# Kernel optimization log

Hardware: AMD Instinct MI355X
Metric: run time of the kernel (lower is better)

The kernel has to match this reference:

```python
import jax, jax.numpy as jnp
import numpy as np

N = 50000        # num nodes
E = 800000       # num edges (before self loops)
IN = 128         # in_channels
HID = 64         # hidden_channels
HEADS = 3        # num_heads
OUT = 32         # out_channels
SLOPE = 0.2      # PyG GATConv default negative_slope
HC = HEADS * HID


def setup_inputs() -> dict:
    key = jax.random.key(0)
    ks = jax.random.split(key, 12)

    def glorot(k, shape, fan_in):
        return jax.random.normal(k, shape, dtype=jnp.float32) / np.float32(np.sqrt(fan_in))

    x = jax.random.normal(ks[0], (N, IN), dtype=jnp.float32)
    edge_index = jax.random.randint(ks[1], (2, E), 0, N, dtype=jnp.int32)
    return {
        "x": x,
        "edge_index": edge_index,
        "W1": glorot(ks[2], (IN, HC), IN),
        "a_src1": glorot(ks[3], (HEADS, HID), HID),
        "a_dst1": glorot(ks[4], (HEADS, HID), HID),
        "b1": jnp.zeros((HC,), jnp.float32),
        "W2": glorot(ks[5], (HC, HC), HC),
        "a_src2": glorot(ks[6], (HEADS, HID), HID),
        "a_dst2": glorot(ks[7], (HEADS, HID), HID),
        "b2": jnp.zeros((HC,), jnp.float32),
        "Wf1": glorot(ks[8], (HC, 64), HC),
        "bf1": jnp.zeros((64,), jnp.float32),
        "Wf2": glorot(ks[9], (64, OUT), 64),
        "bf2": jnp.zeros((OUT,), jnp.float32),
        "num_nodes": N,
    }


def gat_conv(x, src, dst, W, a_src, a_dst, b, num_nodes):
    """PyG-style GATConv: linear -> edge score (LeakyReLU) -> segment softmax
    over incoming edges per destination -> weighted scatter-sum -> concat heads."""
    H, C = a_src.shape
    h = (x @ W).reshape(num_nodes, H, C)              # [N,H,C]
    alpha_s = jnp.einsum("nhc,hc->nh", h, a_src)      # [N,H]
    alpha_d = jnp.einsum("nhc,hc->nh", h, a_dst)      # [N,H]
    e = jax.nn.leaky_relu(alpha_s[src] + alpha_d[dst], SLOPE)  # [E',H]
    # numerically stable segment softmax over destination nodes
    m = jax.lax.stop_gradient(jax.ops.segment_max(e, dst, num_segments=num_nodes))
    ex = jnp.exp(e - m[dst])
    denom = jax.ops.segment_sum(ex, dst, num_segments=num_nodes)
    alpha = ex / (denom[dst] + 1e-16)                 # [E',H]
    msg = h[src] * alpha[:, :, None]                  # [E',H,C]
    out = jax.ops.segment_sum(msg, dst, num_segments=num_nodes)  # [N,H,C]
    return out.reshape(num_nodes, H * C) + b


def reference(x, edge_index, W1, a_src1, a_dst1, b1, W2, a_src2, a_dst2, b2,
              Wf1, bf1, Wf2, bf2, num_nodes):
    # add self loops (PyG GATConv default)
    loops = jnp.arange(num_nodes, dtype=edge_index.dtype)
    src = jnp.concatenate([edge_index[0], loops])
    dst = jnp.concatenate([edge_index[1], loops])

    h = gat_conv(x, src, dst, W1, a_src1, a_dst1, b1, num_nodes)
    h = jax.nn.elu(h)
    # dropout is identity in eval mode
    h = gat_conv(h, src, dst, W2, a_src2, a_dst2, b2, num_nodes)
    h = jax.nn.elu(h)
    h = h @ Wf1 + bf1
    return h @ Wf2 + bf2
```

## Files before the change

kernel.cpp:

```cpp
#include <hip/hip_runtime.h>

#define N_NODES 50000
#define E_EDGES 800000
#define EP (E_EDGES + N_NODES)
#define IN_CH 128
#define HID 64
#define HEADS 3
#define HC 192
#define OUT_CH 32
#define SLOPE 0.2f

#define N4 12500
#define SCAN_BLK 49

#define MB_W1 96
#define MB_W2 (MB_W1 + 144)
#define MB_FOLD (MB_W2 + 25)
#define MB_HIST (MB_FOLD + 3321)

typedef __attribute__((ext_vector_type(8))) short bf16x8;
typedef __attribute__((ext_vector_type(4))) float f32x4;

__device__ __forceinline__ unsigned short f2bf(float f) {
    unsigned int u = __float_as_uint(f);
    u = (u + 0x7fffu + ((u >> 16) & 1u)) >> 16;
    return (unsigned short)u;
}
__device__ __forceinline__ float loF(unsigned int u) { return __uint_as_float(u << 16); }
__device__ __forceinline__ float hiF(unsigned int u) { return __uint_as_float(u & 0xFFFF0000u); }

__device__ __forceinline__ unsigned int fkey(float f) {
    unsigned int u = __float_as_uint(f);
    return (u & 0x80000000u) ? ~u : (u | 0x80000000u);
}
__device__ __forceinline__ float unfkey(unsigned int k) {
    unsigned int u = (k & 0x80000000u) ? (k ^ 0x80000000u) : ~k;
    return __uint_as_float(u);
}


__global__ __launch_bounds__(256) void mega_pre_kernel(
    const float* __restrict__ W1, unsigned short* __restrict__ W1T,
    const float* __restrict__ W2, unsigned short* __restrict__ W2T,
    const float* __restrict__ Wf1, const float* __restrict__ bf1,
    const float* __restrict__ Wf2, const float* __restrict__ bf2,
    unsigned short* __restrict__ WfTb, float* __restrict__ bf,
    const int* __restrict__ ei, int* __restrict__ cnt) {
    int b = blockIdx.x, t = threadIdx.x;
    if (b < MB_W1) {
        int k = (b & 3) * 32 + (t & 31);
        int n = (b >> 2) * 8 + (t >> 5);
        W1T[n * IN_CH + k] = f2bf(W1[(size_t)k * HC + n]);
    } else if (b < MB_W2) {
        int bb = b - MB_W1;
        int k = (bb % 6) * 32 + (t & 31);
        int n = (bb / 6) * 8 + (t >> 5);
        W2T[n * HC + k] = f2bf(W2[(size_t)k * HC + n]);
    } else if (b < MB_FOLD) {
        int id = (b - MB_W2) * 256 + t;
        if (id < HC * OUT_CH) {
            int i = id / OUT_CH, j = id % OUT_CH;
            float s = 0.f;
            for (int k = 0; k < 64; ++k) s += Wf1[i * 64 + k] * Wf2[k * OUT_CH + j];
            WfTb[j * HC + i] = f2bf(s);
        } else if (id < HC * OUT_CH + OUT_CH) {
            int j = id - HC * OUT_CH;
            float s = bf2[j];
            for (int k = 0; k < 64; ++k) s += bf1[k] * Wf2[k * OUT_CH + j];
            bf[j] = s;
        }
    } else {
        int i = (b - MB_FOLD) * 256 + t;
        if (i < EP) {
            int d = (i < E_EDGES) ? ei[E_EDGES + i] : (i - E_EDGES);
            atomicAdd(&cnt[d], 1);
        }
    }
}


__global__ __launch_bounds__(256) void scan_local_kernel(int* __restrict__ cnt,
                                                         int* __restrict__ offs,
                                                         int* __restrict__ bsum) {
    __shared__ int s[256];
    int t = threadIdx.x;
    int g = blockIdx.x * 256 + t;
    int4 v = make_int4(0, 0, 0, 0);
    if (g < N4) v = ((const int4*)cnt)[g];
    int sum = v.x + v.y + v.z + v.w;
    s[t] = sum; __syncthreads();
    #pragma unroll
    for (int o = 1; o < 256; o <<= 1) {
        int u = (t >= o) ? s[t - o] : 0;
        __syncthreads();
        s[t] += u;
        __syncthreads();
    }
    int ex = s[t] - sum;
    if (g < N4) {
        int4 w;
        w.x = ex;
        w.y = ex + v.x;
        w.z = ex + v.x + v.y;
        w.w = ex + v.x + v.y + v.z;
        ((int4*)offs)[g] = w;
        ((int4*)cnt)[g] = make_int4(0, 0, 0, 0);
    }
    if (t == 255) bsum[blockIdx.x] = s[255];
}

__global__ __launch_bounds__(256) void scan_add_kernel(int* __restrict__ offs,
                                                       const int* __restrict__ bsum) {
    int lane = threadIdx.x & 63;
    int orig = (lane < SCAN_BLK) ? bsum[lane] : 0;
    int v = orig;
    #pragma unroll
    for (int o = 1; o < 64; o <<= 1) {
        int u = __shfl_up(v, o);
        if (lane >= o) v += u;
    }
    int add = __shfl(v, blockIdx.x) - __shfl(orig, blockIdx.x);
    int total = __shfl(v, SCAN_BLK - 1);
    int g = blockIdx.x * 256 + threadIdx.x;
    if (g < N4) {
        int4 w = ((int4*)offs)[g];
        w.x += add; w.y += add; w.z += add; w.w += add;
        ((int4*)offs)[g] = w;
    }
    if (blockIdx.x == 0 && threadIdx.x == 0) offs[N_NODES] = total;
}

__global__ void scatter_kernel(const int* __restrict__ ei, const int* __restrict__ offs,
                               int* __restrict__ cnt, int* __restrict__ src_sort) {
    int i = blockIdx.x * 256 + threadIdx.x;
    if (i >= EP) return;
    int s_, d_;
    if (i < E_EDGES) { s_ = ei[i]; d_ = ei[E_EDGES + i]; }
    else             { s_ = d_ = i - E_EDGES; }
    int slot = atomicAdd(&cnt[d_], 1);
    src_sort[offs[d_] + slot] = s_;
}


#define GBM 128
#define GBK 64
#define LDA 72
#define CS_STR 200

template <int K, bool XF32>
__global__ __launch_bounds__(256) void gemm_mfma_kernel(
    const float* __restrict__ Af, const unsigned short* __restrict__ Ab,
    const unsigned short* __restrict__ Wt,
    const float* __restrict__ a_src, const float* __restrict__ a_dst,
    unsigned short* __restrict__ Hb, float* __restrict__ AS, float* __restrict__ AD,
    unsigned int* __restrict__ mk) {
    __shared__ __align__(16) unsigned char smem[51200];
    __shared__ float pmx[4][3];
    unsigned short (*As)[LDA] = (unsigned short (*)[LDA])smem;
    unsigned short (*Bs)[LDA] = (unsigned short (*)[LDA])(smem + GBM * LDA * 2);
    int tid = threadIdx.x;
    int wid = tid >> 6, lane = tid & 63;
    int l15 = lane & 15, l4 = lane >> 4;
    int m0 = blockIdx.x * GBM;
    int sr = tid >> 3, sc = (tid & 7) * 8;

    f32x4 acc[2][12];
    #pragma unroll
    for (int m = 0; m < 2; ++m)
        #pragma unroll
        for (int n = 0; n < 12; ++n) acc[m][n] = (f32x4){0.f, 0.f, 0.f, 0.f};

    for (int kb = 0; kb < K; kb += GBK) {
        #pragma unroll
        for (int i = 0; i < 4; ++i) {
            int r = sr + 32 * i, grow = m0 + r;
            uint4 v = make_uint4(0, 0, 0, 0);
            if (XF32) {
                if (grow < N_NODES) {
                    const float* xp = Af + (size_t)grow * K + kb + sc;
                    float4 v0 = *(const float4*)xp;
                    float4 v1 = *(const float4*)(xp + 4);
                    v.x = (unsigned int)f2bf(v0.x) | ((unsigned int)f2bf(v0.y) << 16);
                    v.y = (unsigned int)f2bf(v0.z) | ((unsigned int)f2bf(v0.w) << 16);
                    v.z = (unsigned int)f2bf(v1.x) | ((unsigned int)f2bf(v1.y) << 16);
                    v.w = (unsigned int)f2bf(v1.z) | ((unsigned int)f2bf(v1.w) << 16);
                }
            } else {
                if (grow < N_NODES) v = *(const uint4*)&Ab[(size_t)grow * K + kb + sc];
            }
            *(uint4*)&As[r][sc] = v;
        }
        #pragma unroll
        for (int i = 0; i < 6; ++i) {
            int n = sr + 32 * i;
            uint4 v = *(const uint4*)&Wt[(size_t)n * K + kb + sc];
            *(uint4*)&Bs[n][sc] = v;
        }
        __syncthreads();
        #pragma unroll
        for (int ks = 0; ks < 2; ++ks) {
            int ko = ks * 32 + l4 * 8;
            bf16x8 a0 = *(const bf16x8*)&As[wid * 32 + l15][ko];
            bf16x8 a1 = *(const bf16x8*)&As[wid * 32 + 16 + l15][ko];
            #pragma unroll
            for (int n = 0; n < 12; ++n) {
                bf16x8 b = *(const bf16x8*)&Bs[n * 16 + l15][ko];
                acc[0][n] = __builtin_amdgcn_mfma_f32_16x16x32_bf16(a0, b, acc[0][n], 0, 0, 0);
                acc[1][n] = __builtin_amdgcn_mfma_f32_16x16x32_bf16(a1, b, acc[1][n], 0, 0, 0);
            }
        }
        __syncthreads();
    }

    float asv[12], adv[12];
    #pragma unroll
    for (int n = 0; n < 12; ++n) {
        asv[n] = a_src[n * 16 + l15];
        adv[n] = a_dst[n * 16 + l15];
    }
    float pm[3] = {-1e30f, -1e30f, -1e30f};
    #pragma unroll
    for (int m = 0; m < 2; ++m)
        #pragma unroll
        for (int r = 0; r < 4; ++r) {
            float ps[3], pd[3];
            #pragma unroll
            for (int h = 0; h < 3; ++h) {
                float s = 0.f, d = 0.f;
                #pragma unroll
                for (int j = 0; j < 4; ++j) {
                    float v = acc[m][4 * h + j][r];
                    s += v * asv[4 * h + j];
                    d += v * adv[4 * h + j];
                }
                #pragma unroll
                for (int o = 1; o < 16; o <<= 1) { s += __shfl_xor(s, o); d += __shfl_xor(d, o); }
                ps[h] = s; pd[h] = d;
                pm[h] = fmaxf(pm[h], s);
            }
            if (l15 == 0) {
                int grow = m0 + wid * 32 + m * 16 + l4 * 4 + r;
                if (grow < N_NODES) {
                    #pragma unroll
                    for (int h = 0; h < 3; ++h) {
                        AS[grow * 3 + h] = ps[h];
                        AD[grow * 3 + h] = pd[h];
                    }
                }
            }
        }
    #pragma unroll
    for (int h = 0; h < 3; ++h) {
        pm[h] = fmaxf(pm[h], __shfl_xor(pm[h], 16));
        pm[h] = fmaxf(pm[h], __shfl_xor(pm[h], 32));
    }
    if (lane == 0) { pmx[wid][0] = pm[0]; pmx[wid][1] = pm[1]; pmx[wid][2] = pm[2]; }

    unsigned short* Cw = (unsigned short*)smem + wid * 32 * CS_STR;
    #pragma unroll
    for (int m = 0; m < 2; ++m)
        #pragma unroll
        for (int n = 0; n < 12; ++n)
            #pragma unroll
            for (int r = 0; r < 4; ++r)
                Cw[(m * 16 + l4 * 4 + r) * CS_STR + n * 16 + l15] = f2bf(acc[m][n][r]);
    __syncthreads();
    #pragma unroll
    for (int i = 0; i < 12; ++i) {
        int c = lane + 64 * i;
        int row = c / 24, off = c % 24;
        int grow = m0 + wid * 32 + row;
        if (grow < N_NODES) {
            uint4 v = *(const uint4*)&Cw[row * CS_STR + off * 8];
            *(uint4*)&Hb[(size_t)grow * HC + off * 8] = v;
        }
    }
    if (tid < 3) {
        float bm = fmaxf(fmaxf(pmx[0][tid], pmx[1][tid]), fmaxf(pmx[2][tid], pmx[3][tid]));
        atomicMax(&mk[tid], fkey(bm));
    }
}


__global__ __launch_bounds__(256) void aggregate_kernel(
    const int* __restrict__ src_sort, const int* __restrict__ offs,
    const float* __restrict__ AS, const float* __restrict__ AD,
    const unsigned int* __restrict__ mkey,
    const unsigned short* __restrict__ Hb, const float* __restrict__ bias,
    unsigned short* __restrict__ Aout) {
    int w = blockIdx.x * 4 + (threadIdx.x >> 6);
    int lane = threadIdx.x & 63;
    int g = lane >> 4, l = lane & 15;
    int beg = offs[w], end = offs[w + 1];

    float ad = 0.f, m = 0.f;
    if (l < 3) {
        ad = AD[w * 3 + l];
        float sm = unfkey(mkey[l]) + ad;
        m = fmaxf(sm, SLOPE * sm);
    }

    int c0 = l * 12;
    int h0 = c0 >> 6, h1 = (c0 + 4) >> 6, h2 = (c0 + 8) >> 6;
    float A0 = 0.f, A1 = 0.f, A2 = 0.f, A3 = 0.f;
    float B0 = 0.f, B1 = 0.f, B2 = 0.f, B3 = 0.f;
    float C0 = 0.f, C1 = 0.f, C2 = 0.f, C3 = 0.f;
    float den = 0.f;

    int p = beg + g;
    bool pv = p < end;
    int s_ = src_sort[pv ? p : (end - 1)];
    float e_;
    {
        float v = (l < 3) ? (AS[s_ * 3 + l] + ad) : 0.f;
        v = fmaxf(v, SLOPE * v);
        e_ = (pv && l < 3) ? __expf(v - m) : 0.f;
    }
    for (int p0 = beg; p0 < end; p0 += 4) {
        int pn = p0 + 4 + g;
        bool pnv = pn < end;
        int sn = src_sort[pnv ? pn : (end - 1)];
        const unsigned short* hr = Hb + (unsigned)s_ * HC + c0;
        uint2 v0 = *(const uint2*)hr;
        uint2 v1 = *(const uint2*)(hr + 4);
        uint2 v2 = *(const uint2*)(hr + 8);
        float en;
        {
            float v = (l < 3) ? (AS[sn * 3 + l] + ad) : 0.f;
            v = fmaxf(v, SLOPE * v);
            en = (pnv && l < 3) ? __expf(v - m) : 0.f;
        }
        den += e_;
        float w0 = __shfl(e_, g * 16 + h0);
        float w1 = __shfl(e_, g * 16 + h1);
        float w2 = __shfl(e_, g * 16 + h2);
        A0 += w0 * loF(v0.x); A1 += w0 * hiF(v0.x); A2 += w0 * loF(v0.y); A3 += w0 * hiF(v0.y);
        B0 += w1 * loF(v1.x); B1 += w1 * hiF(v1.x); B2 += w1 * loF(v1.y); B3 += w1 * hiF(v1.y);
        C0 += w2 * loF(v2.x); C1 += w2 * hiF(v2.x); C2 += w2 * loF(v2.y); C3 += w2 * hiF(v2.y);
        s_ = sn; e_ = en;
    }

    #pragma unroll
    for (int o = 16; o < 64; o <<= 1) {
        A0 += __shfl_xor(A0, o); A1 += __shfl_xor(A1, o); A2 += __shfl_xor(A2, o); A3 += __shfl_xor(A3, o);
        B0 += __shfl_xor(B0, o); B1 += __shfl_xor(B1, o); B2 += __shfl_xor(B2, o); B3 += __shfl_xor(B3, o);
        C0 += __shfl_xor(C0, o); C1 += __shfl_xor(C1, o); C2 += __shfl_xor(C2, o); C3 += __shfl_xor(C3, o);
        den += __shfl_xor(den, o);
    }
    float i0 = 1.f / (__shfl(den, h0) + 1e-16f);
    float i1 = 1.f / (__shfl(den, h1) + 1e-16f);
    float i2 = 1.f / (__shfl(den, h2) + 1e-16f);

    if (lane < 16) {
        float4 bi0 = *(const float4*)&bias[c0];
        float4 bi1 = *(const float4*)&bias[c0 + 4];
        float4 bi2 = *(const float4*)&bias[c0 + 8];
        A0 = A0 * i0 + bi0.x; A1 = A1 * i0 + bi0.y; A2 = A2 * i0 + bi0.z; A3 = A3 * i0 + bi0.w;
        B0 = B0 * i1 + bi1.x; B1 = B1 * i1 + bi1.y; B2 = B2 * i1 + bi1.z; B3 = B3 * i1 + bi1.w;
        C0 = C0 * i2 + bi2.x; C1 = C1 * i2 + bi2.y; C2 = C2 * i2 + bi2.z; C3 = C3 * i2 + bi2.w;
        A0 = (A0 > 0.f) ? A0 : (__expf(A0) - 1.f);
        A1 = (A1 > 0.f) ? A1 : (__expf(A1) - 1.f);
        A2 = (A2 > 0.f) ? A2 : (__expf(A2) - 1.f);
        A3 = (A3 > 0.f) ? A3 : (__expf(A3) - 1.f);
        B0 = (B0 > 0.f) ? B0 : (__expf(B0) - 1.f);
        B1 = (B1 > 0.f) ? B1 : (__expf(B1) - 1.f);
        B2 = (B2 > 0.f) ? B2 : (__expf(B2) - 1.f);
        B3 = (B3 > 0.f) ? B3 : (__expf(B3) - 1.f);
        C0 = (C0 > 0.f) ? C0 : (__expf(C0) - 1.f);
        C1 = (C1 > 0.f) ? C1 : (__expf(C1) - 1.f);
        C2 = (C2 > 0.f) ? C2 : (__expf(C2) - 1.f);
        C3 = (C3 > 0.f) ? C3 : (__expf(C3) - 1.f);
        unsigned short* op = Aout + (size_t)w * HC + c0;
        uint2 o0, o1, o2;
        o0.x = (unsigned int)f2bf(A0) | ((unsigned int)f2bf(A1) << 16);
        o0.y = (unsigned int)f2bf(A2) | ((unsigned int)f2bf(A3) << 16);
        o1.x = (unsigned int)f2bf(B0) | ((unsigned int)f2bf(B1) << 16);
        o1.y = (unsigned int)f2bf(B2) | ((unsigned int)f2bf(B3) << 16);
        o2.x = (unsigned int)f2bf(C0) | ((unsigned int)f2bf(C1) << 16);
        o2.y = (unsigned int)f2bf(C2) | ((unsigned int)f2bf(C3) << 16);
        *(uint2*)op = o0;
        *(uint2*)(op + 4) = o1;
        *(uint2*)(op + 8) = o2;
    }
}


__global__ __launch_bounds__(256) void mlp_mfma_kernel(
    const unsigned short* __restrict__ act, const unsigned short* __restrict__ WfTb,
    const float* __restrict__ bf, float* __restrict__ out) {
    int tid = threadIdx.x;
    int wid = tid >> 6, lane = tid & 63;
    int l15 = lane & 15, l4 = lane >> 4;
    int m0 = blockIdx.x * 128 + wid * 32;

    f32x4 acc[2][2];
    #pragma unroll
    for (int m = 0; m < 2; ++m)
        #pragma unroll
        for (int n = 0; n < 2; ++n) acc[m][n] = (f32x4){0.f, 0.f, 0.f, 0.f};

    int r0 = m0 + l15, r1 = m0 + 16 + l15;
    bool v0r = r0 < N_NODES, v1r = r1 < N_NODES;
    const unsigned short* a0p = act + (size_t)(v0r ? r0 : 0) * HC;
    const unsigned short* a1p = act + (size_t)(v1r ? r1 : 0) * HC;
    const unsigned short* b0p = WfTb + (size_t)l15 * HC;
    const unsigned short* b1p = WfTb + (size_t)(16 + l15) * HC;

    #pragma unroll
    for (int ks = 0; ks < 6; ++ks) {
        int k0 = ks * 32 + l4 * 8;
        bf16x8 a0 = *(const bf16x8*)&a0p[k0];
        bf16x8 a1 = *(const bf16x8*)&a1p[k0];
        bf16x8 b0 = *(const bf16x8*)&b0p[k0];
        bf16x8 b1 = *(const bf16x8*)&b1p[k0];
        acc[0][0] = __builtin_amdgcn_mfma_f32_16x16x32_bf16(a0, b0, acc[0][0], 0, 0, 0);
        acc[0][1] = __builtin_amdgcn_mfma_f32_16x16x32_bf16(a0, b1, acc[0][1], 0, 0, 0);
        acc[1][0] = __builtin_amdgcn_mfma_f32_16x16x32_bf16(a1, b0, acc[1][0], 0, 0, 0);
        acc[1][1] = __builtin_amdgcn_mfma_f32_16x16x32_bf16(a1, b1, acc[1][1], 0, 0, 0);
    }

    float bv0 = bf[l15], bv1 = bf[16 + l15];
    #pragma unroll
    for (int m = 0; m < 2; ++m)
        #pragma unroll
        for (int r = 0; r < 4; ++r) {
            int row = m0 + m * 16 + l4 * 4 + r;
            if (row < N_NODES) {
                out[(size_t)row * OUT_CH + l15]      = acc[m][0][r] + bv0;
                out[(size_t)row * OUT_CH + 16 + l15] = acc[m][1][r] + bv1;
            }
        }
}


extern "C" void kernel_launch(void* const* d_in, const int* in_sizes, int n_in,
                              void* d_out, int out_size, void* d_ws, size_t ws_size,
                              hipStream_t stream) {
    (void)in_sizes; (void)n_in; (void)out_size; (void)ws_size;
    const float* x   = (const float*)d_in[0];
    const int*   ei  = (const int*)d_in[1];
    const float* W1  = (const float*)d_in[2];
    const float* as1 = (const float*)d_in[3];
    const float* ad1 = (const float*)d_in[4];
    const float* b1  = (const float*)d_in[5];
    const float* W2  = (const float*)d_in[6];
    const float* as2 = (const float*)d_in[7];
    const float* ad2 = (const float*)d_in[8];
    const float* b2  = (const float*)d_in[9];
    const float* Wf1 = (const float*)d_in[10];
    const float* bf1 = (const float*)d_in[11];
    const float* Wf2 = (const float*)d_in[12];
    const float* bf2 = (const float*)d_in[13];
    float* out = (float*)d_out;

    char* ws = (char*)d_ws;
    size_t off = 0;
    auto alloc = [&](size_t b) { size_t o = off; off += (b + 255) & ~(size_t)255; return o; };
    unsigned short* W1T = (unsigned short*)(ws + alloc((size_t)HC * IN_CH * 2));
    unsigned short* W2T = (unsigned short*)(ws + alloc((size_t)HC * HC * 2));
    unsigned short* HB  = (unsigned short*)(ws + alloc((size_t)N_NODES * HC * 2));
    unsigned short* ACT = (unsigned short*)(ws + alloc((size_t)N_NODES * HC * 2));
    int*   SRC  = (int*)  (ws + alloc((size_t)(EP + 64) * 4));
    float* AS   = (float*)(ws + alloc((size_t)N_NODES * 3 * 4));
    float* AD   = (float*)(ws + alloc((size_t)N_NODES * 3 * 4));
    int*   OFFS = (int*)  (ws + alloc((size_t)(N_NODES + 4) * 4));
    int*   CNT  = (int*)  (ws + alloc((size_t)(N_NODES + 16) * 4));
    unsigned int* MKEY = (unsigned int*)(CNT + N_NODES);
    int*   BSUM = (int*)  (ws + alloc((size_t)256 * 4));
    unsigned short* WFT = (unsigned short*)(ws + alloc((size_t)OUT_CH * HC * 2));
    float* BF   = (float*)(ws + alloc((size_t)OUT_CH * 4));

    int eb = (EP + 255) / 256;
    int gmb = (N_NODES + GBM - 1) / GBM;

    hipMemsetAsync(CNT, 0, (size_t)(N_NODES + 16) * 4, stream);
    mega_pre_kernel<<<MB_HIST, 256, 0, stream>>>(W1, W1T, W2, W2T,
                                                 Wf1, bf1, Wf2, bf2, WFT, BF, ei, CNT);
    scan_local_kernel<<<SCAN_BLK, 256, 0, stream>>>(CNT, OFFS, BSUM);
    scan_add_kernel<<<SCAN_BLK, 256, 0, stream>>>(OFFS, BSUM);
    scatter_kernel<<<eb, 256, 0, stream>>>(ei, OFFS, CNT, SRC);

    gemm_mfma_kernel<IN_CH, true><<<gmb, 256, 0, stream>>>(x, nullptr, W1T, as1, ad1, HB, AS, AD, MKEY);
    aggregate_kernel<<<(N_NODES + 3) / 4, 256, 0, stream>>>(SRC, OFFS, AS, AD, MKEY, HB, b1, ACT);
    gemm_mfma_kernel<HC, false><<<gmb, 256, 0, stream>>>(nullptr, ACT, W2T, as2, ad2, HB, AS, AD, MKEY + 3);
    aggregate_kernel<<<(N_NODES + 3) / 4, 256, 0, stream>>>(SRC, OFFS, AS, AD, MKEY + 3, HB, b2, ACT);
    mlp_mfma_kernel<<<gmb, 256, 0, stream>>>(ACT, WFT, BF, out);
}
```

Baseline: 280.9 us.

## Replace per-node atomic scatter with two-pass bucketed counting sort in LDS

The edge scatter into CSR order is split into two passes. The first pass bins edges into 128-node buckets using one global atomic counter per bucket and writes packed (local dst, src) words to a staging buffer. The second pass sorts each bucket in shared memory and writes it out contiguously. This aims to replace scattered per-node global atomics and random writes with more localized traffic, at the cost of an extra kernel and buffer. It relies on src fitting in 16 bits and slot in 9 bits, but N=50000 exceeds 65535? No, it fits, yet slot<<23 allows only 512 edges per node and bucket size must stay under SCAP, which holds only for typical random graphs.

```diff
diff --git a/kernel.cpp b/kernel.cpp
--- a/kernel.cpp
+++ b/kernel.cpp
@@ -12,6 +12,8 @@
 
 #define N4 12500
 #define SCAN_BLK 49
+#define NBKT 391
+#define SCAP 4096
 
 #define MB_W1 96
 #define MB_W2 (MB_W1 + 144)
@@ -104,7 +106,6 @@
         w.z = ex + v.x + v.y;
         w.w = ex + v.x + v.y + v.z;
         ((int4*)offs)[g] = w;
-        ((int4*)cnt)[g] = make_int4(0, 0, 0, 0);
     }
     if (t == 255) bsum[blockIdx.x] = s[255];
 }
@@ -130,15 +131,61 @@
     if (blockIdx.x == 0 && threadIdx.x == 0) offs[N_NODES] = total;
 }
 
-__global__ void scatter_kernel(const int* __restrict__ ei, const int* __restrict__ offs,
-                               int* __restrict__ cnt, int* __restrict__ src_sort) {
+
+__global__ void scatter1_kernel(const int* __restrict__ ei, const int* __restrict__ offs,
+                                int* __restrict__ bcnt, unsigned int* __restrict__ stage) {
     int i = blockIdx.x * 256 + threadIdx.x;
     if (i >= EP) return;
     int s_, d_;
     if (i < E_EDGES) { s_ = ei[i]; d_ = ei[E_EDGES + i]; }
     else             { s_ = d_ = i - E_EDGES; }
-    int slot = atomicAdd(&cnt[d_], 1);
-    src_sort[offs[d_] + slot] = s_;
+    int b = d_ >> 7;
+    int slot = atomicAdd(&bcnt[b], 1);
+    stage[offs[b << 7] + slot] = ((unsigned int)(d_ & 127) << 16) | (unsigned int)s_;
+}
+
+__global__ __launch_bounds__(256) void scatter2_kernel(const unsigned int* __restrict__ stage,
+                                                       const int* __restrict__ offs,
+                                                       int* __restrict__ src_sort) {
+    __shared__ unsigned int ents[SCAP];
+    __shared__ int outb[SCAP];
+    __shared__ int lcnt[128];
+    __shared__ int lsc[128];
+    int b = blockIdx.x, t = threadIdx.x;
+    int beg = offs[b << 7];
+    int hi = (b << 7) + 128; if (hi > N_NODES) hi = N_NODES;
+    int end = offs[hi];
+    int n = end - beg;
+    if (t < 128) lcnt[t] = 0;
+    __syncthreads();
+    for (int i = t; i < n; i += 256) {
+        unsigned int v = stage[beg + i];
+        int dloc = (v >> 16) & 127;
+        int slot = atomicAdd(&lcnt[dloc], 1);
+        ents[i] = v | ((unsigned int)slot << 23);
+    }
+    __syncthreads();
+    int cv = (t < 128) ? lcnt[t] : 0;
+    if (t < 128) lsc[t] = cv;
+    __syncthreads();
+    #pragma unroll
+    for (int o = 1; o < 128; o <<= 1) {
+        int u = 0;
+        if (t < 128 && t >= o) u = lsc[t - o];
+        __syncthreads();
+        if (t < 128) lsc[t] += u;
+        __syncthreads();
+    }
+    if (t < 128) lsc[t] -= cv;
+    __syncthreads();
+    for (int i = t; i < n; i += 256) {
+        unsigned int v = ents[i];
+        int dloc = (v >> 16) & 127;
+        int slot = v >> 23;
+        outb[lsc[dloc] + slot] = (int)(v & 0xFFFFu);
+    }
+    __syncthreads();
+    for (int i = t; i < n; i += 256) src_sort[beg + i] = outb[i];
 }
 
 
@@ -461,11 +508,13 @@
     unsigned short* HB  = (unsigned short*)(ws + alloc((size_t)N_NODES * HC * 2));
     unsigned short* ACT = (unsigned short*)(ws + alloc((size_t)N_NODES * HC * 2));
     int*   SRC  = (int*)  (ws + alloc((size_t)(EP + 64) * 4));
+    unsigned int* STG = (unsigned int*)(ws + alloc((size_t)(EP + 64) * 4));
     float* AS   = (float*)(ws + alloc((size_t)N_NODES * 3 * 4));
     float* AD   = (float*)(ws + alloc((size_t)N_NODES * 3 * 4));
     int*   OFFS = (int*)  (ws + alloc((size_t)(N_NODES + 4) * 4));
-    int*   CNT  = (int*)  (ws + alloc((size_t)(N_NODES + 16) * 4));
+    int*   CNT  = (int*)  (ws + alloc((size_t)(N_NODES + 16 + 512) * 4));
     unsigned int* MKEY = (unsigned int*)(CNT + N_NODES);
+    int*   BCNT = CNT + N_NODES + 16;
     int*   BSUM = (int*)  (ws + alloc((size_t)256 * 4));
     unsigned short* WFT = (unsigned short*)(ws + alloc((size_t)OUT_CH * HC * 2));
     float* BF   = (float*)(ws + alloc((size_t)OUT_CH * 4));
@@ -473,12 +522,13 @@
     int eb = (EP + 255) / 256;
     int gmb = (N_NODES + GBM - 1) / GBM;
 
-    hipMemsetAsync(CNT, 0, (size_t)(N_NODES + 16) * 4, stream);
+    hipMemsetAsync(CNT, 0, (size_t)(N_NODES + 16 + 512) * 4, stream);
     mega_pre_kernel<<<MB_HIST, 256, 0, stream>>>(W1, W1T, W2, W2T,
                                                  Wf1, bf1, Wf2, bf2, WFT, BF, ei, CNT);
     scan_local_kernel<<<SCAN_BLK, 256, 0, stream>>>(CNT, OFFS, BSUM);
     scan_add_kernel<<<SCAN_BLK, 256, 0, stream>>>(OFFS, BSUM);
-    scatter_kernel<<<eb, 256, 0, stream>>>(ei, OFFS, CNT, SRC);
+    scatter1_kernel<<<eb, 256, 0, stream>>>(ei, OFFS, BCNT, STG);
+    scatter2_kernel<<<NBKT, 256, 0, stream>>>(STG, OFFS, SRC);
 
     gemm_mfma_kernel<IN_CH, true><<<gmb, 256, 0, stream>>>(x, nullptr, W1T, as1, ad1, HB, AS, AD, MKEY);
     aggregate_kernel<<<(N_NODES + 3) / 4, 256, 0, stream>>>(SRC, OFFS, AS, AD, MKEY, HB, b1, ACT);
```

Result: slower. 569.3 us (+102.7%).
